# Optimization experiments

Hardware: AMD Instinct MI355X
Metric: run time of the kernel (lower is better)

The kernel has to match this reference:

```python
import jax, jax.numpy as jnp
import numpy as np

HIDDEN = 2048
N_HEADS = 32
N_KV_HEADS = 8
HEAD_DIM = 64
ROPE_THETA = 500000.0
B, S = 1, 2048


def _rope_tables(seq_len):
    inv_freq = 1.0 / ROPE_THETA ** (jnp.arange(0, HEAD_DIM, 2, dtype=jnp.float32) / HEAD_DIM)
    angles = jnp.arange(seq_len, dtype=jnp.float32)[:, None] * inv_freq[None, :]
    return jnp.cos(angles), jnp.sin(angles)


def _apply_rope(x, cos, sin):
    # x: (B, S, H, D); cos/sin: (S, D//2)
    x1 = x[..., 0::2]
    x2 = x[..., 1::2]
    c = cos[None, :, None, :]
    s = sin[None, :, None, :]
    x1r = x1 * c - x2 * s
    x2r = x1 * s + x2 * c
    return jnp.stack([x1r, x2r], axis=-1).reshape(x.shape)


def setup_inputs() -> dict:
    key = jax.random.key(0)
    ks = jax.random.split(key, 5)
    hidden_states = jax.random.normal(ks[0], (B, S, HIDDEN), dtype=jnp.float32)
    # causal mask, broadcastable over (B, H, S, S)
    attention_mask = jnp.tril(jnp.ones((S, S), dtype=bool))[None, :, :]
    sc = 1.0 / np.sqrt(HIDDEN)
    wq = jax.random.normal(ks[1], (HIDDEN, N_HEADS * HEAD_DIM), dtype=jnp.float32) * sc
    wk = jax.random.normal(ks[2], (HIDDEN, N_KV_HEADS * HEAD_DIM), dtype=jnp.float32) * sc
    wv = jax.random.normal(ks[3], (HIDDEN, N_KV_HEADS * HEAD_DIM), dtype=jnp.float32) * sc
    wo = jax.random.normal(ks[4], (N_HEADS * HEAD_DIM, HIDDEN), dtype=jnp.float32) * sc
    return {"hidden_states": hidden_states, "attention_mask": attention_mask,
            "wq": wq, "wk": wk, "wv": wv, "wo": wo}


def reference(hidden_states, attention_mask, wq, wk, wv, wo):
    b, s, _ = hidden_states.shape
    groups = N_HEADS // N_KV_HEADS
    q = (hidden_states @ wq).reshape(b, s, N_HEADS, HEAD_DIM)
    k = (hidden_states @ wk).reshape(b, s, N_KV_HEADS, HEAD_DIM)
    v = (hidden_states @ wv).reshape(b, s, N_KV_HEADS, HEAD_DIM)
    cos, sin = _rope_tables(s)
    q = _apply_rope(q, cos, sin)
    k = _apply_rope(k, cos, sin)
    k = jnp.repeat(k, groups, axis=2)  # (b, s, H, D)
    v = jnp.repeat(v, groups, axis=2)
    q = q.transpose(0, 2, 1, 3)  # (b, H, s, D)
    k = k.transpose(0, 2, 1, 3)
    v = v.transpose(0, 2, 1, 3)
    scores = jnp.einsum('bhqd,bhkd->bhqk', q, k) / jnp.sqrt(jnp.float32(HEAD_DIM))
    scores = jnp.where(attention_mask[:, None, :, :], scores, -jnp.inf)
    probs = jax.nn.softmax(scores, axis=-1)
    out = jnp.einsum('bhqk,bhkd->bhqd', probs, v)
    out = out.transpose(0, 2, 1, 3).reshape(b, s, N_HEADS * HEAD_DIM)
    return out @ wo
```

## Files before the change

### kernel.cpp

```cpp
#include <hip/hip_runtime.h>

typedef __attribute__((ext_vector_type(8))) short short8;
typedef __attribute__((ext_vector_type(4))) float float4v;

union U4S8 { uint4 u; short8 s; };

__device__ __forceinline__ float bf2f(ushort u) {
    union { uint i; float f; } v; v.i = ((uint)u) << 16; return v.f;
}
__device__ __forceinline__ ushort f2bf(float f) {
    union { uint i; float f; } v; v.f = f;
    return (ushort)((v.i + 0x7FFFu + ((v.i >> 16) & 1u)) >> 16);
}
#if __has_builtin(__builtin_amdgcn_cvt_pk_bf16_f32)
__device__ __forceinline__ uint f2bf_pk(float a, float b) {
    auto r = __builtin_amdgcn_cvt_pk_bf16_f32(a, b);
    return __builtin_bit_cast(uint, r);
}
#else
__device__ __forceinline__ uint f2bf_pk(float a, float b) {
    return (uint)f2bf(a) | ((uint)f2bf(b) << 16);
}
#endif
__device__ __forceinline__ void gld_lds16(const ushort* g, ushort* l) {
    __builtin_amdgcn_global_load_lds((const __attribute__((address_space(1))) unsigned int*)g,
                                     (__attribute__((address_space(3))) unsigned int*)l,
                                     16, 0, 0);
}

__device__ __forceinline__ void tconv_body(const float* in, ushort* out,
                                           int C, int r0, int c0, int tid) {
    __shared__ float t[64][65];
    const int lrow = tid >> 2;
    const int lc   = (tid & 3) * 16;
    const float* ip = in + (size_t)(r0 + lrow) * C + c0 + lc;
#pragma unroll
    for (int i = 0; i < 4; i++) {
        float4 v = *(const float4*)(ip + 4 * i);
        t[lrow][lc + 4 * i + 0] = v.x; t[lrow][lc + 4 * i + 1] = v.y;
        t[lrow][lc + 4 * i + 2] = v.z; t[lrow][lc + 4 * i + 3] = v.w;
    }
    __syncthreads();
    ushort* op = out + (size_t)(c0 + lrow) * 2048 + r0 + lc;
#pragma unroll
    for (int i = 0; i < 8; i++)
        ((uint*)op)[i] = f2bf_pk(t[lc + 2 * i][lrow], t[lc + 2 * i + 1][lrow]);
}

__global__ __launch_bounds__(256) void prep(const float* __restrict__ hidden,
                                            const float* __restrict__ wq,
                                            const float* __restrict__ wk,
                                            const float* __restrict__ wv,
                                            const float* __restrict__ wo,
                                            ushort* __restrict__ hid,
                                            ushort* __restrict__ wT,
                                            ushort* __restrict__ woT) {
    const int bx = blockIdx.x;
    if (bx < 2048) {
        const size_t i = ((size_t)bx * 256 + threadIdx.x) * 8;
        float4 a = *(const float4*)(hidden + i);
        float4 b = *(const float4*)(hidden + i + 4);
        uint4 u;
        u.x = f2bf_pk(a.x, a.y); u.y = f2bf_pk(a.z, a.w);
        u.z = f2bf_pk(b.x, b.y); u.w = f2bf_pk(b.z, b.w);
        *(uint4*)(hid + i) = u;
    } else if (bx < 3584) {
        const int i = bx - 2048;
        const int xx = i % 48, yy = i / 48;
        const float* in; ushort* op; int C, cx;
        if (xx < 32)      { in = wq; op = wT;                        C = 2048; cx = xx; }
        else if (xx < 40) { in = wk; op = wT + (size_t)2048 * 2048;  C = 512;  cx = xx - 32; }
        else              { in = wv; op = wT + (size_t)2560 * 2048;  C = 512;  cx = xx - 40; }
        tconv_body(in, op, C, yy * 64, cx * 64, threadIdx.x);
    } else {
        const int i = bx - 3584;
        tconv_body(wo, woT, 2048, (i >> 5) * 64, (i & 31) * 64, threadIdx.x);
    }
}

template <bool BF16OUT>
__global__ __launch_bounds__(256) void gemm_n64(const ushort* __restrict__ A,
                                                const ushort* __restrict__ Bt,
                                                void* __restrict__ Cout,
                                                int N, int K, int lda, int ropeQKV) {
    __shared__ ushort As[2][128 * 32];
    __shared__ ushort Bs[2][64 * 32];

    const int tid = threadIdx.x, w = tid >> 6, lane = tid & 63;
    const int lr = lane & 15, quad = lane >> 4;
    const int m0 = blockIdx.x * 128, n0 = blockIdx.y * 64;

    const int srow = lane >> 2;
    const int skb  = (lane & 3) ^ ((srow >> 1) & 3);

    const ushort* Ap = A  + (size_t)(m0 + srow) * lda + skb * 8;
    const ushort* Bp = Bt + (size_t)(n0 + w * 16 + srow) * K + skb * 8;

    float4v acc[2][4];
#pragma unroll
    for (int a = 0; a < 2; a++)
#pragma unroll
        for (int b = 0; b < 4; b++) { acc[a][b][0] = 0.f; acc[a][b][1] = 0.f; acc[a][b][2] = 0.f; acc[a][b][3] = 0.f; }

    const int fsw = (lr >> 1) & 3;

#pragma unroll
    for (int i = 0; i < 2; i++) {
        const int rt = 2 * w + i;
        gld_lds16(Ap + (size_t)(rt * 16) * lda, &As[0][rt * 512]);
    }
    gld_lds16(Bp, &Bs[0][w * 512]);

    const int niter = K >> 5;
    for (int it = 0; it < niter; it++) {
        const int b = it & 1;

        asm volatile("s_waitcnt vmcnt(0) lgkmcnt(0)\n\ts_barrier" ::: "memory");

        if (it + 1 < niter) {
            const int k1 = (it + 1) << 5;
#pragma unroll
            for (int i = 0; i < 2; i++) {
                const int rt = 2 * w + i;
                gld_lds16(Ap + (size_t)(rt * 16) * lda + k1, &As[1 - b][rt * 512]);
            }
            gld_lds16(Bp + k1, &Bs[1 - b][w * 512]);
        }

        short8 af[2], bf[4];
#pragma unroll
        for (int mt = 0; mt < 2; mt++)
            af[mt] = *(const short8*)&As[b][(w * 32 + mt * 16 + lr) * 32 + (quad ^ fsw) * 8];
#pragma unroll
        for (int nt = 0; nt < 4; nt++)
            bf[nt] = *(const short8*)&Bs[b][(nt * 16 + lr) * 32 + (quad ^ fsw) * 8];
#pragma unroll
        for (int mt = 0; mt < 2; mt++)
#pragma unroll
            for (int nt = 0; nt < 4; nt++)
                acc[mt][nt] = __builtin_amdgcn_mfma_f32_16x16x32_bf16(af[mt], bf[nt], acc[mt][nt], 0, 0, 0);
    }

    const int rbase = m0 + w * 32 + quad * 4;
    const int cbase = n0 + lr;
    if (BF16OUT) {
        ushort* Cb = (ushort*)Cout;
        if (ropeQKV && (int)blockIdx.y < 40) {
            const float osc = ((int)blockIdx.y < 32) ? 0.18033688f : 1.0f;
            const float sgn = (lr & 1) ? 1.0f : -1.0f;
#pragma unroll
            for (int nt = 0; nt < 4; nt++) {
                const int col = cbase + nt * 16;
                const int j = (col >> 1) & 31;
                const float inv = __expf(-(float)(2 * j) * (1.0f / 64.0f) * 13.122363377404328f);
#pragma unroll
                for (int mt = 0; mt < 2; mt++)
#pragma unroll
                    for (int r = 0; r < 4; r++) {
                        const int row = rbase + mt * 16 + r;
                        float sn, cs;
                        sincosf((float)row * inv, &sn, &cs);
                        const float mine = acc[mt][nt][r];
                        const float partner = __shfl_xor(mine, 1);
                        Cb[(size_t)row * N + col] = f2bf((mine * cs + sgn * partner * sn) * osc);
                    }
            }
        } else {
#pragma unroll
            for (int mt = 0; mt < 2; mt++)
#pragma unroll
                for (int nt = 0; nt < 4; nt++)
#pragma unroll
                    for (int r = 0; r < 4; r++)
                        Cb[(size_t)(rbase + mt * 16 + r) * N + cbase + nt * 16] = f2bf(acc[mt][nt][r]);
        }
    } else {
        float* Cf = (float*)Cout;
#pragma unroll
        for (int mt = 0; mt < 2; mt++)
#pragma unroll
            for (int nt = 0; nt < 4; nt++)
#pragma unroll
                for (int r = 0; r < 4; r++)
                    Cf[(size_t)(rbase + mt * 16 + r) * N + cbase + nt * 16] = acc[mt][nt][r];
    }
}

__global__ __launch_bounds__(256) void attn_mfma(const ushort* __restrict__ Q,
                                                 const ushort* __restrict__ Kc,
                                                 const ushort* __restrict__ Vc,
                                                 ushort* __restrict__ O0,
                                                 ushort* __restrict__ O1,
                                                 float* __restrict__ L0,
                                                 float* __restrict__ L1) {
    __shared__ ushort Ks[2][64 * 64];
    __shared__ ushort Vt[2][64 * 64];
    __shared__ ushort Ps[4][16 * 64];

    const int tid = threadIdx.x, w = tid >> 6, lane = tid & 63;
    const int lr = lane & 15, quad = lane >> 4;
    const int h = blockIdx.y, g = h >> 2, z = blockIdx.z;

    const int dg = tid & 15;
    const int kl = tid >> 4;
    const int ksub = lane >> 3, dsub = lane & 7;
    ushort* Pw = Ps[w];
    ushort* Op = z ? O1 : O0;
    float*  Lp = z ? L1 : L0;

    const ushort* Vp0 = Vc + g * 64 + dg * 4 + (size_t)3072 * kl;
    const ushort* Kp0 = Kc + g * 64 + ((dsub ^ ksub) * 8) + (size_t)3072 * ksub;

    short8 onesf;
#pragma unroll
    for (int j = 0; j < 8; j++) onesf[j] = (short)0x3F80;

    for (int ti = 0; ti < 2; ti++) {
        const int bx = ti ? 31 - (int)blockIdx.x : (int)blockIdx.x;
        const int nch = (bx >= z) ? ((bx - z) >> 1) + 1 : 0;
        const int last = z + 2 * (nch - 1);

        const ushort* qp = Q + (size_t)(bx * 64 + w * 16 + lr) * 3072 + h * 64 + quad * 8;
        const short8 qf0 = *(const short8*)qp;
        const short8 qf1 = *(const short8*)(qp + 32);

        float4v oacc[4], lacc;
#pragma unroll
        for (int t = 0; t < 4; t++) { oacc[t][0] = 0.f; oacc[t][1] = 0.f; oacc[t][2] = 0.f; oacc[t][3] = 0.f; }
        lacc[0] = 0.f; lacc[1] = 0.f; lacc[2] = 0.f; lacc[3] = 0.f;

        uint2 vv[4];
        if (nch) {
#pragma unroll
            for (int t = 0; t < 4; t++)
                vv[t] = *(const uint2*)(Vp0 + (size_t)(z * 64 + 16 * t) * 3072);
        }
        __syncthreads();
        if (nch) {
#pragma unroll
            for (int i = 0; i < 2; i++) {
                const int rt = 2 * w + i;
                gld_lds16(Kp0 + (size_t)(z * 64 + rt * 8) * 3072, &Ks[0][rt * 512]);
            }
        }

        for (int c = 0; c < nch; c++) {
            const int kb = z + 2 * c;
            const int b = c & 1;
            ushort* bKs = Ks[b];
            ushort* bVt = Vt[b];

#pragma unroll
            for (int i = 0; i < 4; i++) {
                const uint sel = (i & 1) ? 0x07060302u : 0x05040100u;
                uint s0 = (i < 2) ? vv[0].x : vv[0].y;
                uint s1 = (i < 2) ? vv[1].x : vv[1].y;
                uint s2 = (i < 2) ? vv[2].x : vv[2].y;
                uint s3 = (i < 2) ? vv[3].x : vv[3].y;
                uint2 pk;
                pk.x = __builtin_amdgcn_perm(s1, s0, sel);
                pk.y = __builtin_amdgcn_perm(s3, s2, sel);
                *(uint2*)&bVt[(dg * 4 + i) * 64 + (kl ^ ((dg & 3) * 4 + i)) * 4] = pk;
            }

            const int kn = (c + 1 < nch) ? kb + 2 : last;
#pragma unroll
            for (int t = 0; t < 4; t++)
                vv[t] = *(const uint2*)(Vp0 + (size_t)(kn * 64 + 16 * t) * 3072);

            asm volatile("s_waitcnt vmcnt(4) lgkmcnt(0)\n\ts_barrier" ::: "memory");

#pragma unroll
            for (int i = 0; i < 2; i++) {
                const int rt = 2 * w + i;
                gld_lds16(Kp0 + (size_t)(kn * 64 + rt * 8) * 3072, &Ks[1 - b][rt * 512]);
            }

            float4v sacc[4];
#pragma unroll
            for (int t = 0; t < 4; t++) { sacc[t][0] = 0.f; sacc[t][1] = 0.f; sacc[t][2] = 0.f; sacc[t][3] = 0.f; }
#pragma unroll
            for (int t = 0; t < 4; t++) {
                const int krow = t * 16 + lr;
                const int sw = lr & 7;
                short8 kf0 = *(const short8*)&bKs[krow * 64 + ((quad)     ^ sw) * 8];
                short8 kf1 = *(const short8*)&bKs[krow * 64 + ((quad + 4) ^ sw) * 8];
                sacc[t] = __builtin_amdgcn_mfma_f32_16x16x32_bf16(qf0, kf0, sacc[t], 0, 0, 0);
                sacc[t] = __builtin_amdgcn_mfma_f32_16x16x32_bf16(qf1, kf1, sacc[t], 0, 0, 0);
            }

            if (kb == bx) {
#pragma unroll
                for (int r = 0; r < 4; r++) {
                    const int qr = w * 16 + quad * 4 + r;
                    float p0 = exp2f(sacc[0][r]), p1 = exp2f(sacc[1][r]);
                    float p2 = exp2f(sacc[2][r]), p3 = exp2f(sacc[3][r]);
                    if (lr > qr)      p0 = 0.f;
                    if (16 + lr > qr) p1 = 0.f;
                    if (32 + lr > qr) p2 = 0.f;
                    if (48 + lr > qr) p3 = 0.f;
                    const int prow = quad * 4 + r;
                    uint2 pk; pk.x = f2bf_pk(p0, p1); pk.y = f2bf_pk(p2, p3);
                    *(uint2*)&Pw[prow * 64 + (lr ^ prow) * 4] = pk;
                }
            } else {
#pragma unroll
                for (int r = 0; r < 4; r++) {
                    const int prow = quad * 4 + r;
                    uint2 pk;
                    pk.x = f2bf_pk(exp2f(sacc[0][r]), exp2f(sacc[1][r]));
                    pk.y = f2bf_pk(exp2f(sacc[2][r]), exp2f(sacc[3][r]));
                    *(uint2*)&Pw[prow * 64 + (lr ^ prow) * 4] = pk;
                }
            }

#pragma unroll
            for (int ks2 = 0; ks2 < 2; ks2++) {
                const int ub = ks2 * 8 + quad * 2;
                U4S8 pu;
                uint2 plo = *(const uint2*)&Pw[lr * 64 + ((ub)     ^ lr) * 4];
                uint2 phi = *(const uint2*)&Pw[lr * 64 + ((ub + 1) ^ lr) * 4];
                pu.u.x = plo.x; pu.u.y = plo.y; pu.u.z = phi.x; pu.u.w = phi.y;
                lacc = __builtin_amdgcn_mfma_f32_16x16x32_bf16(pu.s, onesf, lacc, 0, 0, 0);
#pragma unroll
                for (int t = 0; t < 4; t++) {
                    const int d = t * 16 + lr;
                    U4S8 vu;
                    uint2 vlo = *(const uint2*)&bVt[d * 64 + ((ub)     ^ lr) * 4];
                    uint2 vhi = *(const uint2*)&bVt[d * 64 + ((ub + 1) ^ lr) * 4];
                    vu.u.x = vlo.x; vu.u.y = vlo.y; vu.u.z = vhi.x; vu.u.w = vhi.y;
                    oacc[t] = __builtin_amdgcn_mfma_f32_16x16x32_bf16(pu.s, vu.s, oacc[t], 0, 0, 0);
                }
            }
        }

        ushort* op = Op + (size_t)(bx * 64 + w * 16 + quad * 4) * 2048 + h * 64 + lr;
#pragma unroll
        for (int t = 0; t < 4; t++)
#pragma unroll
            for (int r = 0; r < 4; r++)
                op[(size_t)r * 2048 + t * 16] = f2bf(oacc[t][r]);
        if (lr == 0) {
#pragma unroll
            for (int r = 0; r < 4; r++)
                Lp[h * 2048 + bx * 64 + w * 16 + quad * 4 + r] = lacc[r];
        }
    }
}

__global__ __launch_bounds__(256) void combine(ushort* __restrict__ O0,
                                               const ushort* __restrict__ O1,
                                               const float* __restrict__ L0,
                                               const float* __restrict__ L1) {
    const int idx = blockIdx.x * 256 + threadIdx.x;
    const int r = idx >> 8;
    const int c8 = (idx & 255) * 8;
    const int h = c8 >> 6;
    const float rl = 1.0f / (L0[h * 2048 + r] + L1[h * 2048 + r]);
    uint4 a = *(const uint4*)(O0 + (size_t)r * 2048 + c8);
    uint4 b = *(const uint4*)(O1 + (size_t)r * 2048 + c8);
    uint ua[4] = {a.x, a.y, a.z, a.w}, ub[4] = {b.x, b.y, b.z, b.w};
    uint rr[4];
#pragma unroll
    for (int k = 0; k < 4; k++) {
        float x0 = bf2f((ushort)(ua[k] & 0xFFFFu)) + bf2f((ushort)(ub[k] & 0xFFFFu));
        float x1 = bf2f((ushort)(ua[k] >> 16))     + bf2f((ushort)(ub[k] >> 16));
        rr[k] = f2bf_pk(x0 * rl, x1 * rl);
    }
    uint4 res; res.x = rr[0]; res.y = rr[1]; res.z = rr[2]; res.w = rr[3];
    *(uint4*)(O0 + (size_t)r * 2048 + c8) = res;
}

extern "C" void kernel_launch(void* const* d_in, const int* in_sizes, int n_in,
                              void* d_out, int out_size, void* d_ws, size_t ws_size,
                              hipStream_t stream) {
    const float* hidden = (const float*)d_in[0];
    const float* wq = (const float*)d_in[2];
    const float* wk = (const float*)d_in[3];
    const float* wv = (const float*)d_in[4];
    const float* wo = (const float*)d_in[5];

    ushort* ws = (ushort*)d_ws;
    ushort* hid = ws;
    ushort* wT  = ws + 4194304;
    ushort* woT = ws + 10485760;
    ushort* O1  = wT;
    float*  L0  = (float*)(ws + 8388608);
    float*  L1  = L0 + 65536;
    ushort* QKV = (ushort*)d_out;

    prep<<<4608, 256, 0, stream>>>(hidden, wq, wk, wv, wo, hid, wT, woT);
    gemm_n64<true><<<dim3(16, 48), 256, 0, stream>>>(hid, wT, QKV, 3072, 2048, 2048, 1);
    attn_mfma<<<dim3(16, 32, 2), 256, 0, stream>>>(QKV, QKV + 2048, QKV + 2560,
                                                   hid , O1, L0, L1);
    combine<<<2048, 256, 0, stream>>>(hid, O1, L0, L1);
    gemm_n64<false><<<dim3(16, 32), 256, 0, stream>>>(hid, woT, d_out, 2048, 2048, 2048, 0);
}
```

Baseline: 239.1 us.

## Widen GEMM block tile to 128x128 with 8 waves in a 4x2 grid

The projection GEMMs now use 128x128 output tiles computed by 512-thread blocks, with waves laid out 4 rows by 2 columns. Each wave loads one 16-row slice of A and of B into LDS, which halves the grid size and doubles reuse of each staged A tile across output columns. The RoPE and scale block-index thresholds are rescaled for the new tile width. The cost is fewer blocks: 384 and 256 on a chip with many CUs, which may leave CUs underused.

```diff
diff --git a/kernel.cpp b/kernel.cpp
--- a/kernel.cpp
+++ b/kernel.cpp
@@ -79,22 +79,23 @@
 }
 
 template <bool BF16OUT>
-__global__ __launch_bounds__(256) void gemm_n64(const ushort* __restrict__ A,
-                                                const ushort* __restrict__ Bt,
-                                                void* __restrict__ Cout,
-                                                int N, int K, int lda, int ropeQKV) {
+__global__ __launch_bounds__(512, 4) void gemm_n128(const ushort* __restrict__ A,
+                                                    const ushort* __restrict__ Bt,
+                                                    void* __restrict__ Cout,
+                                                    int N, int K, int lda, int ropeQKV) {
     __shared__ ushort As[2][128 * 32];
-    __shared__ ushort Bs[2][64 * 32];
+    __shared__ ushort Bs[2][128 * 32];
 
     const int tid = threadIdx.x, w = tid >> 6, lane = tid & 63;
     const int lr = lane & 15, quad = lane >> 4;
-    const int m0 = blockIdx.x * 128, n0 = blockIdx.y * 64;
+    const int m0 = blockIdx.x * 128, n0 = blockIdx.y * 128;
+    const int wr = w >> 1, wc = w & 1;
 
     const int srow = lane >> 2;
     const int skb  = (lane & 3) ^ ((srow >> 1) & 3);
 
-    const ushort* Ap = A  + (size_t)(m0 + srow) * lda + skb * 8;
-    const ushort* Bp = Bt + (size_t)(n0 + w * 16 + srow) * K + skb * 8;
+    const ushort* Ap = A  + (size_t)(m0 + 16 * w + srow) * lda + skb * 8;
+    const ushort* Bp = Bt + (size_t)(n0 + 16 * w + srow) * K + skb * 8;
 
     float4v acc[2][4];
 #pragma unroll
@@ -103,15 +104,11 @@
         for (int b = 0; b < 4; b++) { acc[a][b][0] = 0.f; acc[a][b][1] = 0.f; acc[a][b][2] = 0.f; acc[a][b][3] = 0.f; }
 
     const int fsw = (lr >> 1) & 3;
-
-#pragma unroll
-    for (int i = 0; i < 2; i++) {
-        const int rt = 2 * w + i;
-        gld_lds16(Ap + (size_t)(rt * 16) * lda, &As[0][rt * 512]);
-    }
+    const int niter = K >> 5;
+
+    gld_lds16(Ap, &As[0][w * 512]);
     gld_lds16(Bp, &Bs[0][w * 512]);
 
-    const int niter = K >> 5;
     for (int it = 0; it < niter; it++) {
         const int b = it & 1;
 
@@ -119,21 +116,17 @@
 
         if (it + 1 < niter) {
             const int k1 = (it + 1) << 5;
-#pragma unroll
-            for (int i = 0; i < 2; i++) {
-                const int rt = 2 * w + i;
-                gld_lds16(Ap + (size_t)(rt * 16) * lda + k1, &As[1 - b][rt * 512]);
-            }
+            gld_lds16(Ap + k1, &As[1 - b][w * 512]);
             gld_lds16(Bp + k1, &Bs[1 - b][w * 512]);
         }
 
         short8 af[2], bf[4];
 #pragma unroll
         for (int mt = 0; mt < 2; mt++)
-            af[mt] = *(const short8*)&As[b][(w * 32 + mt * 16 + lr) * 32 + (quad ^ fsw) * 8];
+            af[mt] = *(const short8*)&As[b][(wr * 32 + mt * 16 + lr) * 32 + (quad ^ fsw) * 8];
 #pragma unroll
         for (int nt = 0; nt < 4; nt++)
-            bf[nt] = *(const short8*)&Bs[b][(nt * 16 + lr) * 32 + (quad ^ fsw) * 8];
+            bf[nt] = *(const short8*)&Bs[b][(wc * 64 + nt * 16 + lr) * 32 + (quad ^ fsw) * 8];
 #pragma unroll
         for (int mt = 0; mt < 2; mt++)
 #pragma unroll
@@ -141,12 +134,12 @@
                 acc[mt][nt] = __builtin_amdgcn_mfma_f32_16x16x32_bf16(af[mt], bf[nt], acc[mt][nt], 0, 0, 0);
     }
 
-    const int rbase = m0 + w * 32 + quad * 4;
-    const int cbase = n0 + lr;
+    const int rbase = m0 + wr * 32 + quad * 4;
+    const int cbase = n0 + wc * 64 + lr;
     if (BF16OUT) {
         ushort* Cb = (ushort*)Cout;
-        if (ropeQKV && (int)blockIdx.y < 40) {
-            const float osc = ((int)blockIdx.y < 32) ? 0.18033688f : 1.0f;
+        if (ropeQKV && (int)blockIdx.y < 20) {
+            const float osc = ((int)blockIdx.y < 16) ? 0.18033688f : 1.0f;
             const float sgn = (lr & 1) ? 1.0f : -1.0f;
 #pragma unroll
             for (int nt = 0; nt < 4; nt++) {
@@ -390,9 +383,9 @@
     ushort* QKV = (ushort*)d_out;
 
     prep<<<4608, 256, 0, stream>>>(hidden, wq, wk, wv, wo, hid, wT, woT);
-    gemm_n64<true><<<dim3(16, 48), 256, 0, stream>>>(hid, wT, QKV, 3072, 2048, 2048, 1);
+    gemm_n128<true><<<dim3(16, 24), 512, 0, stream>>>(hid, wT, QKV, 3072, 2048, 2048, 1);
     attn_mfma<<<dim3(16, 32, 2), 256, 0, stream>>>(QKV, QKV + 2048, QKV + 2560,
                                                    hid , O1, L0, L1);
     combine<<<2048, 256, 0, stream>>>(hid, O1, L0, L1);
-    gemm_n64<false><<<dim3(16, 32), 256, 0, stream>>>(hid, woT, d_out, 2048, 2048, 2048, 0);
-}
+    gemm_n128<false><<<dim3(16, 16), 512, 0, stream>>>(hid, woT, d_out, 2048, 2048, 2048, 0);
+}
```

New measurement: 245.6 us. 1.03x slower.
